# Kernel tuning notes

Measured on AMD Instinct MI355X. Metric: run time of the kernel, lower is better.

## Reference

```python
import jax, jax.numpy as jnp
import numpy as np

EPS_LN = 1e-5

def _layernorm(x, g, b):
    mu = jnp.mean(x, axis=-1, keepdims=True)
    var = jnp.mean((x - mu) ** 2, axis=-1, keepdims=True)
    return (x - mu) * jax.lax.rsqrt(var + EPS_LN) * g + b

def _act_quant_ste(x):
    # clip_val uses detached stats -> stop_gradient
    clip_val = jax.lax.stop_gradient(
        jnp.clip(jnp.mean(jnp.abs(x), axis=-1, keepdims=True), 1e-8, None)) * 2.5
    scale = clip_val / 127.0
    x_scaled = x / scale
    x_clip = jnp.clip(x_scaled, -127.0, 127.0)
    x_q = x_scaled + jax.lax.stop_gradient(jnp.round(x_clip) - x_scaled)
    return x_q * scale

def _weight_quant_ste(w):
    scale = jax.lax.stop_gradient(jnp.clip(jnp.mean(jnp.abs(w)), 1e-8, None))
    w_norm = w / scale
    w_clip = jnp.clip(w_norm, -1.0, 1.0)
    w_q = w_norm + jax.lax.stop_gradient(jnp.round(w_clip) - w_norm)
    return w_q * scale

def _bitlinear(x, w, g, b):
    # w: [out, in]; x: [B,T,in]
    x_q = _act_quant_ste(_layernorm(x, g, b))
    w_q = _weight_quant_ste(w)
    return jnp.einsum('btd,hd->bth', x_q, w_q)

def setup_inputs() -> dict:
    D, H = 2048, 2048 * 4
    B, T = 4, 2048
    key = jax.random.key(0)
    ks = jax.random.split(key, 4)
    std = 0.02
    return {
        'x': jax.random.normal(ks[0], (B, T, D), dtype=jnp.float32),
        'mu_k': jnp.zeros((1, 1, D), jnp.float32),
        'mu_r': jnp.zeros((1, 1, D), jnp.float32),
        'wk': jax.random.normal(ks[1], (H, D), jnp.float32) * std,
        'gk': jnp.ones((D,), jnp.float32), 'bk': jnp.zeros((D,), jnp.float32),
        'wr': jax.random.normal(ks[2], (D, D), jnp.float32) * std,
        'gr': jnp.ones((D,), jnp.float32), 'br': jnp.zeros((D,), jnp.float32),
        'wv': jax.random.normal(ks[3], (D, H), jnp.float32) * std,
        'gv': jnp.ones((H,), jnp.float32), 'bv': jnp.zeros((H,), jnp.float32),
    }

def reference(x, mu_k, mu_r, wk, gk, bk, wr, gr, br, wv, gv, bv):
    B, T, C = x.shape
    prev = jnp.zeros((B, 1, C), dtype=x.dtype)  # state=None path
    x_prev = jnp.concatenate([prev, x[:, :-1, :]], axis=1)  # token shift
    dx = x_prev - x
    k_act = jax.nn.relu(_bitlinear(x + dx * mu_k, wk, gk, bk)) ** 2  # [B,T,H]
    rgate = jax.nn.sigmoid(_bitlinear(x + dx * mu_r, wr, gr, br))    # [B,T,D]
    out = rgate * _bitlinear(k_act, wv, gv, bv)                      # [B,T,D]
    return out, jax.lax.stop_gradient(x[:, -1:, :])
```

## Files before the change

### kernel.cpp

```cpp
#include <hip/hip_runtime.h>

#define T_LEN 2048
#define B_SZ  4
#define D_DIM 2048
#define H_DIM 8192
#define BT    (B_SZ * T_LEN)

typedef float f32x4 __attribute__((ext_vector_type(4)));
typedef int   i32x4v __attribute__((ext_vector_type(4)));
typedef int   i32x16v __attribute__((ext_vector_type(16)));

__device__ __forceinline__ float block_sum(float v, float* red) {
    #pragma unroll
    for (int o = 32; o > 0; o >>= 1) v += __shfl_down(v, o, 64);
    const int lane = threadIdx.x & 63, w = threadIdx.x >> 6;
    if (lane == 0) red[w] = v;
    __syncthreads();
    float r = red[0] + red[1] + red[2] + red[3];
    __syncthreads();
    return r;
}

__global__ void wabs_partial(const float* __restrict__ w, int n,
                             float* __restrict__ part) {
    __shared__ float red[16];
    float s = 0.f;
    int i = (blockIdx.x * 256 + threadIdx.x) * 8;
    const int stride = gridDim.x * 256 * 8;
    for (; i < n; i += stride) {
        f32x4 a = *(const f32x4*)(w + i);
        f32x4 b = *(const f32x4*)(w + i + 4);
        #pragma unroll
        for (int j = 0; j < 4; j++) s += fabsf(a[j]) + fabsf(b[j]);
    }
    float tot = block_sum(s, red);
    if (threadIdx.x == 0) part[blockIdx.x] = tot;
}

__global__ void wfinal(const float* __restrict__ part, int nparts, int n,
                       float* __restrict__ outp) {
    __shared__ float red[16];
    float s = 0.f;
    for (int i = threadIdx.x; i < nparts; i += 256) s += part[i];
    float tot = block_sum(s, red);
    if (threadIdx.x == 0) outp[0] = fmaxf(tot / (float)n, 1e-8f);
}

__global__ void wquant(const float* __restrict__ w, const float* __restrict__ sp,
                       signed char* __restrict__ q, int n) {
    const float s = *sp;
    int i = (blockIdx.x * 256 + threadIdx.x) * 16;
    const int stride = gridDim.x * 256 * 16;
    for (; i < n; i += stride) {
        union { signed char c[16]; i32x4v v; } pk;
        #pragma unroll
        for (int h = 0; h < 4; h++) {
            f32x4 a = *(const f32x4*)(w + i + h * 4);
            #pragma unroll
            for (int j = 0; j < 4; j++)
                pk.c[h * 4 + j] =
                    (signed char)(int)rintf(fminf(fmaxf(a[j] / s, -1.f), 1.f));
        }
        *(i32x4v*)(q + i) = pk.v;
    }
}

__device__ __forceinline__ void ln_quant8(const float* xm_in,
                                          const float* __restrict__ g,
                                          const float* __restrict__ b,
                                          signed char* qrow, float* srow, float* red) {
    const int base = threadIdx.x * 8;
    float xm[8];
    float s = 0.f;
    #pragma unroll
    for (int j = 0; j < 8; j++) { xm[j] = xm_in[j]; s += xm[j]; }
    const float mean = block_sum(s, red) * (1.f / D_DIM);
    float s2 = 0.f;
    #pragma unroll
    for (int j = 0; j < 8; j++) { float d = xm[j] - mean; s2 += d * d; }
    const float var  = block_sum(s2, red) * (1.f / D_DIM);
    const float rstd = 1.f / sqrtf(var + 1e-5f);
    f32x4 ga = *(const f32x4*)(g + base), gb = *(const f32x4*)(g + base + 4);
    f32x4 ba = *(const f32x4*)(b + base), bb2 = *(const f32x4*)(b + base + 4);
    float gg[8] = {ga[0],ga[1],ga[2],ga[3],gb[0],gb[1],gb[2],gb[3]};
    float bb[8] = {ba[0],ba[1],ba[2],ba[3],bb2[0],bb2[1],bb2[2],bb2[3]};
    float sa = 0.f;
    #pragma unroll
    for (int j = 0; j < 8; j++) {
        xm[j] = (xm[j] - mean) * rstd * gg[j] + bb[j];
        sa += fabsf(xm[j]);
    }
    const float amean = block_sum(sa, red) * (1.f / D_DIM);
    const float scale = fmaxf(amean, 1e-8f) * 2.5f / 127.0f;
    union { signed char c[8]; int2 v; } pk;
    #pragma unroll
    for (int j = 0; j < 8; j++)
        pk.c[j] = (signed char)(int)rintf(fminf(fmaxf(xm[j] / scale, -127.f), 127.f));
    *(int2*)(qrow + base) = pk.v;
    if (threadIdx.x == 0) *srow = scale;
}

__global__ void act_prep(const float* __restrict__ x, int row0,
                         const float* __restrict__ muk,
                         const float* __restrict__ gk, const float* __restrict__ bk,
                         const float* __restrict__ mur,
                         const float* __restrict__ gr, const float* __restrict__ br,
                         signed char* __restrict__ qk, float* __restrict__ sk,
                         signed char* __restrict__ qr, float* __restrict__ sr,
                         float* __restrict__ out2) {
    __shared__ float red[16];
    const int lrow = blockIdx.x;
    const int row = row0 + lrow;
    const int t = row & (T_LEN - 1);
    const int base = threadIdx.x * 8;

    float xv[8], xp[8];
    f32x4 xa = *(const f32x4*)(x + (size_t)row * D_DIM + base);
    f32x4 xb = *(const f32x4*)(x + (size_t)row * D_DIM + base + 4);
    xv[0]=xa[0]; xv[1]=xa[1]; xv[2]=xa[2]; xv[3]=xa[3];
    xv[4]=xb[0]; xv[5]=xb[1]; xv[6]=xb[2]; xv[7]=xb[3];
    if (t > 0) {
        f32x4 pa = *(const f32x4*)(x + (size_t)(row - 1) * D_DIM + base);
        f32x4 pb = *(const f32x4*)(x + (size_t)(row - 1) * D_DIM + base + 4);
        xp[0]=pa[0]; xp[1]=pa[1]; xp[2]=pa[2]; xp[3]=pa[3];
        xp[4]=pb[0]; xp[5]=pb[1]; xp[6]=pb[2]; xp[7]=pb[3];
    } else {
        #pragma unroll
        for (int j = 0; j < 8; j++) xp[j] = 0.f;
    }
    if (t == T_LEN - 1) {
        const int bb = row / T_LEN;
        *(f32x4*)(out2 + (size_t)bb * D_DIM + base)     = xa;
        *(f32x4*)(out2 + (size_t)bb * D_DIM + base + 4) = xb;
    }
    float mk[8], mr[8], xmk[8], xmr[8];
    f32x4 mka = *(const f32x4*)(muk + base), mkb = *(const f32x4*)(muk + base + 4);
    f32x4 mra = *(const f32x4*)(mur + base), mrb = *(const f32x4*)(mur + base + 4);
    mk[0]=mka[0]; mk[1]=mka[1]; mk[2]=mka[2]; mk[3]=mka[3];
    mk[4]=mkb[0]; mk[5]=mkb[1]; mk[6]=mkb[2]; mk[7]=mkb[3];
    mr[0]=mra[0]; mr[1]=mra[1]; mr[2]=mra[2]; mr[3]=mra[3];
    mr[4]=mrb[0]; mr[5]=mrb[1]; mr[6]=mrb[2]; mr[7]=mrb[3];
    #pragma unroll
    for (int j = 0; j < 8; j++) {
        const float dx = xp[j] - xv[j];
        xmk[j] = xv[j] + dx * mk[j];
        xmr[j] = xv[j] + dx * mr[j];
    }
    ln_quant8(xmk, gk, bk, qk + (size_t)lrow * D_DIM, sk + lrow, red);
    ln_quant8(xmr, gr, br, qr + (size_t)lrow * D_DIM, sr + lrow, red);
}

__global__ void lnq_v(const float* __restrict__ kact,
                      const float* __restrict__ g, const float* __restrict__ b,
                      signed char* __restrict__ qv, float* __restrict__ sv) {
    __shared__ float red[16];
    const int row = blockIdx.x;
    const int base = threadIdx.x * 32;
    const float* kr = kact + (size_t)row * H_DIM + base;

    float v[32];
    float s = 0.f;
    #pragma unroll
    for (int c = 0; c < 8; c++) {
        f32x4 a = *(const f32x4*)(kr + c * 4);
        #pragma unroll
        for (int j = 0; j < 4; j++) { v[c * 4 + j] = a[j]; s += a[j]; }
    }
    const float mean = block_sum(s, red) * (1.f / H_DIM);
    float s2 = 0.f;
    #pragma unroll
    for (int j = 0; j < 32; j++) { float d = v[j] - mean; s2 += d * d; }
    const float var  = block_sum(s2, red) * (1.f / H_DIM);
    const float rstd = 1.f / sqrtf(var + 1e-5f);
    float sa = 0.f;
    #pragma unroll
    for (int c = 0; c < 8; c++) {
        f32x4 ga = *(const f32x4*)(g + base + c * 4);
        f32x4 ba = *(const f32x4*)(b + base + c * 4);
        #pragma unroll
        for (int j = 0; j < 4; j++) {
            int k = c * 4 + j;
            v[k] = (v[k] - mean) * rstd * ga[j] + ba[j];
            sa += fabsf(v[k]);
        }
    }
    const float amean = block_sum(sa, red) * (1.f / H_DIM);
    const float scale = fmaxf(amean, 1e-8f) * 2.5f / 127.0f;
    union { signed char c[32]; i32x4v v4[2]; } pk;
    #pragma unroll
    for (int j = 0; j < 32; j++)
        pk.c[j] = (signed char)(int)rintf(fminf(fmaxf(v[j] / scale, -127.f), 127.f));
    *(i32x4v*)(qv + (size_t)row * H_DIM + base)      = pk.v4[0];
    *(i32x4v*)(qv + (size_t)row * H_DIM + base + 16) = pk.v4[1];
    if (threadIdx.x == 0) sv[row] = scale;
}

template <int EP, int BM, int BN, int WM, int WN>
__global__ __launch_bounds__(512, 2) void gemm8(
    const signed char* __restrict__ A, const signed char* __restrict__ B,
    int K, int Nn, int gn,
    const float* __restrict__ sa, const float* __restrict__ swp,
    const float* __restrict__ gate, float* __restrict__ out_f) {
    constexpr int MT  = BM / WM / 32;
    constexpr int NTC = BN / WN / 32;
    constexpr int ALOADS = BM / 64;
    constexpr int BLOADS = BN / 64;
    constexpr int LOADS  = ALOADS + BLOADS;
    constexpr int L0 = LOADS / 2;

    __shared__ signed char As[2][BM * 128];
    __shared__ signed char Bs[2][BN * 128];

    const int tid = threadIdx.x;
    const int nwg = gridDim.x;
    const int q8  = nwg >> 3;
    const int swz = (blockIdx.x & 7) * q8 + (blockIdx.x >> 3);
    const int bm = swz / gn, bn = swz % gn;

    const int lane = tid & 63, wave = tid >> 6;
    const int wr = wave / WN, wc = wave % WN;
    const int lrow = lane & 31, lhalf = lane >> 5;

    i32x16v acc[MT][NTC] = {};

    const size_t arow0 = (size_t)bm * BM;
    const size_t brow0 = (size_t)bn * BN;
    const int NT = K >> 7;

    auto stage_one = [&](int buf, int k0, int j) {
        if (j < ALOADS) {
            const int o = j * 512 + tid;
            const int r = o >> 3, sl = o & 7;
            const signed char* g = A + (arow0 + r) * (size_t)K + k0 + ((sl ^ (r & 7)) * 16);
            __builtin_amdgcn_global_load_lds(
                (const __attribute__((address_space(1))) void*)g,
                (__attribute__((address_space(3))) void*)(As[buf] + o * 16), 16, 0, 0);
        } else {
            const int o = (j - ALOADS) * 512 + tid;
            const int r = o >> 3, sl = o & 7;
            const signed char* g = B + (brow0 + r) * (size_t)K + k0 + ((sl ^ (r & 7)) * 16);
            __builtin_amdgcn_global_load_lds(
                (const __attribute__((address_space(1))) void*)g,
                (__attribute__((address_space(3))) void*)(Bs[buf] + o * 16), 16, 0, 0);
        }
    };

    auto read_frags = [&](const signed char* AsB, const signed char* BsB, int ks0,
                          i32x4v (&af)[MT][2], i32x4v (&bf)[NTC][2]) {
        #pragma unroll
        for (int s = 0; s < 2; s++) {
            const int slot = (ks0 + s) * 2 + lhalf;
            #pragma unroll
            for (int tm = 0; tm < MT; tm++) {
                const int r = wr * (MT * 32) + tm * 32 + lrow;
                af[tm][s] = *(const i32x4v*)(AsB + r * 128 + ((slot ^ (r & 7)) * 16));
            }
            #pragma unroll
            for (int tn = 0; tn < NTC; tn++) {
                const int r = wc * (NTC * 32) + tn * 32 + lrow;
                bf[tn][s] = *(const i32x4v*)(BsB + r * 128 + ((slot ^ (r & 7)) * 16));
            }
        }
    };

    auto do_mfma = [&](i32x4v (&af)[MT][2], i32x4v (&bf)[NTC][2]) {
        #pragma unroll
        for (int s = 0; s < 2; s++)
            #pragma unroll
            for (int tm = 0; tm < MT; tm++)
                #pragma unroll
                for (int tn = 0; tn < NTC; tn++)
                    acc[tm][tn] = __builtin_amdgcn_mfma_i32_32x32x32_i8(
                        af[tm][s], bf[tn][s], acc[tm][tn], 0, 0, 0);
    };

    #pragma unroll
    for (int j = 0; j < LOADS; j++) stage_one(0, 0, j);

    for (int t = 0; t < NT; t++) {
        const int cur = t & 1;
        const signed char* AsB = As[cur];
        const signed char* BsB = Bs[cur];
        const int kn = (t + 1) << 7;
        const bool pf = (t + 1 < NT);

        if (pf) {
            #pragma unroll
            for (int j = 0; j < L0; j++) stage_one(cur ^ 1, kn, j);
            if constexpr (L0 == 4) asm volatile("s_waitcnt vmcnt(4)" ::: "memory");
            else                   asm volatile("s_waitcnt vmcnt(3)" ::: "memory");
        } else {
            asm volatile("s_waitcnt vmcnt(0)" ::: "memory");
        }
        __builtin_amdgcn_sched_barrier(0);
        __builtin_amdgcn_s_barrier();
        __builtin_amdgcn_sched_barrier(0);
        {
            i32x4v af[MT][2], bf[NTC][2];
            read_frags(AsB, BsB, 0, af, bf);
            __builtin_amdgcn_s_setprio(1);
            do_mfma(af, bf);
            __builtin_amdgcn_s_setprio(0);
        }
        __builtin_amdgcn_sched_barrier(0);
        __builtin_amdgcn_s_barrier();
        {
            i32x4v af[MT][2], bf[NTC][2];
            read_frags(AsB, BsB, 2, af, bf);
            if (pf) {
                #pragma unroll
                for (int j = L0; j < LOADS; j++) stage_one(cur ^ 1, kn, j);
            }
            __builtin_amdgcn_sched_barrier(0);
            __builtin_amdgcn_s_barrier();
            __builtin_amdgcn_sched_barrier(0);
            __builtin_amdgcn_s_setprio(1);
            do_mfma(af, bf);
            __builtin_amdgcn_s_setprio(0);
        }
        __builtin_amdgcn_sched_barrier(0);
        __builtin_amdgcn_s_barrier();
    }

    const float sw = *swp;
    #pragma unroll
    for (int tm = 0; tm < MT; tm++) {
        #pragma unroll
        for (int tn = 0; tn < NTC; tn++) {
            #pragma unroll
            for (int rg = 0; rg < 16; rg++) {
                const int rin  = (rg & 3) + 8 * (rg >> 2) + 4 * lhalf;
                const int grow = bm * BM + wr * (MT * 32) + tm * 32 + rin;
                const int gcol = bn * BN + wc * (NTC * 32) + tn * 32 + lrow;
                const float v = (float)acc[tm][tn][rg] * sa[grow] * sw;
                const size_t idx = (size_t)grow * Nn + gcol;
                if (EP == 0) {
                    float rv = fmaxf(v, 0.f);
                    out_f[idx] = rv * rv;
                } else if (EP == 1) {
                    out_f[idx] = 1.0f / (1.0f + expf(-v));
                } else {
                    out_f[idx] = gate[idx] * v;
                }
            }
        }
    }
}

extern "C" void kernel_launch(void* const* d_in, const int* in_sizes, int n_in,
                              void* d_out, int out_size, void* d_ws, size_t ws_size,
                              hipStream_t stream) {
    const float* x   = (const float*)d_in[0];
    const float* muk = (const float*)d_in[1];
    const float* mur = (const float*)d_in[2];
    const float* wk  = (const float*)d_in[3];
    const float* gk  = (const float*)d_in[4];
    const float* bk  = (const float*)d_in[5];
    const float* wr  = (const float*)d_in[6];
    const float* gr  = (const float*)d_in[7];
    const float* br  = (const float*)d_in[8];
    const float* wv  = (const float*)d_in[9];
    const float* gv  = (const float*)d_in[10];
    const float* bv  = (const float*)d_in[11];

    char* wsb = (char*)d_ws;
    size_t off = 0;
    auto alloc = [&](size_t bytes) -> size_t {
        size_t p = off;
        off = (off + bytes + 255) & ~(size_t)255;
        return p;
    };
    const size_t o_wqk  = alloc((size_t)H_DIM * D_DIM);
    const size_t o_wqr  = alloc((size_t)D_DIM * D_DIM);
    const size_t o_wqv  = alloc((size_t)D_DIM * H_DIM);
    const size_t o_wsc  = alloc(64);
    const size_t o_part = alloc(3 * 1024 * sizeof(float));
    const size_t fixed  = off;

    int CH = BT;
    while (CH > 256 &&
           fixed + (size_t)CH * (D_DIM + D_DIM + H_DIM + 4 * H_DIM + 4 * D_DIM + 12) + 8192 > ws_size)
        CH >>= 1;
    const size_t o_xqk  = alloc((size_t)CH * D_DIM);
    const size_t o_xqr  = alloc((size_t)CH * D_DIM);
    const size_t o_xqv  = alloc((size_t)CH * H_DIM);
    const size_t o_kact = alloc((size_t)CH * H_DIM * 4);
    const size_t o_gate = alloc((size_t)CH * D_DIM * 4);
    const size_t o_sk   = alloc((size_t)CH * 4);
    const size_t o_sr   = alloc((size_t)CH * 4);
    const size_t o_sv   = alloc((size_t)CH * 4);

    signed char* wqk = (signed char*)(wsb + o_wqk);
    signed char* wqr = (signed char*)(wsb + o_wqr);
    signed char* wqv = (signed char*)(wsb + o_wqv);
    float* wsc  = (float*)(wsb + o_wsc);
    float* part = (float*)(wsb + o_part);
    signed char* xqk = (signed char*)(wsb + o_xqk);
    signed char* xqr = (signed char*)(wsb + o_xqr);
    signed char* xqv = (signed char*)(wsb + o_xqv);
    float* kact = (float*)(wsb + o_kact);
    float* gate = (float*)(wsb + o_gate);
    float* sk = (float*)(wsb + o_sk);
    float* sr = (float*)(wsb + o_sr);
    float* sv = (float*)(wsb + o_sv);

    float* outp = (float*)d_out;
    float* out2 = outp + (size_t)BT * D_DIM;

    wabs_partial<<<1024, 256, 0, stream>>>(wk, H_DIM * D_DIM, part + 0 * 1024);
    wabs_partial<<<1024, 256, 0, stream>>>(wr, D_DIM * D_DIM, part + 1 * 1024);
    wabs_partial<<<1024, 256, 0, stream>>>(wv, D_DIM * H_DIM, part + 2 * 1024);
    wfinal<<<1, 256, 0, stream>>>(part + 0 * 1024, 1024, H_DIM * D_DIM, wsc + 0);
    wfinal<<<1, 256, 0, stream>>>(part + 1 * 1024, 1024, D_DIM * D_DIM, wsc + 1);
    wfinal<<<1, 256, 0, stream>>>(part + 2 * 1024, 1024, D_DIM * H_DIM, wsc + 2);
    wquant<<<2048, 256, 0, stream>>>(wk, wsc + 0, wqk, H_DIM * D_DIM);
    wquant<<<2048, 256, 0, stream>>>(wr, wsc + 1, wqr, D_DIM * D_DIM);
    wquant<<<2048, 256, 0, stream>>>(wv, wsc + 2, wqv, D_DIM * H_DIM);

    for (int row0 = 0; row0 < BT; row0 += CH) {
        act_prep<<<CH, 256, 0, stream>>>(x, row0, muk, gk, bk, mur, gr, br,
                                         xqk, sk, xqr, sr, out2);

        gemm8<1, 256, 128, 4, 2><<<(CH / 256) * (D_DIM / 128), 512, 0, stream>>>(
            xqr, wqr, D_DIM, D_DIM, D_DIM / 128, sr, wsc + 1,
            (const float*)nullptr, gate);

        gemm8<0, 256, 256, 2, 4><<<(CH / 256) * (H_DIM / 256), 512, 0, stream>>>(
            xqk, wqk, D_DIM, H_DIM, H_DIM / 256, sk, wsc + 0,
            (const float*)nullptr, kact);

        lnq_v<<<CH, 256, 0, stream>>>(kact, gv, bv, xqv, sv);

        gemm8<2, 256, 128, 4, 2><<<(CH / 256) * (D_DIM / 128), 512, 0, stream>>>(
            xqv, wqv, H_DIM, D_DIM, D_DIM / 128, sv, wsc + 2,
            gate, outp + (size_t)row0 * D_DIM);
    }
}
```

Measured before the change: 740.5 us.

## Store k_act as bf16 and retile the K-projection GEMM with BK=64

The intermediate relu² activation from the K-projection GEMM is now written as bf16 rather than fp32, which halves its write traffic and the read traffic in the following LayerNorm-quantize kernel. The GEMM template gains a BK parameter with a single-stage BK=64 pipeline and a matching LDS swizzle, and the K GEMM moves to 512x128 tiles with 8x1 waves. Chunk sizing now accounts for the smaller buffer and keeps a larger minimum chunk. Rounding k_act to bf16 before LayerNorm and int8 quantization can change some quantized values, and the new tile shape changes occupancy and LDS use.

```diff
diff --git a/kernel.cpp b/kernel.cpp
--- a/kernel.cpp
+++ b/kernel.cpp
@@ -9,6 +9,17 @@
 typedef float f32x4 __attribute__((ext_vector_type(4)));
 typedef int   i32x4v __attribute__((ext_vector_type(4)));
 typedef int   i32x16v __attribute__((ext_vector_type(16)));
+typedef unsigned short ushort8 __attribute__((ext_vector_type(8)));
+
+__device__ __forceinline__ float bf2f(unsigned short u) {
+    unsigned int i = ((unsigned int)u) << 16;
+    return __builtin_bit_cast(float, i);
+}
+__device__ __forceinline__ unsigned short f2bf(float f) {
+    unsigned int i = __builtin_bit_cast(unsigned int, f);
+    i += 0x7fffu + ((i >> 16) & 1u);
+    return (unsigned short)(i >> 16);
+}
 
 __device__ __forceinline__ float block_sum(float v, float* red) {
     #pragma unroll
@@ -150,21 +161,21 @@
     ln_quant8(xmr, gr, br, qr + (size_t)lrow * D_DIM, sr + lrow, red);
 }
 
-__global__ void lnq_v(const float* __restrict__ kact,
+__global__ void lnq_v(const unsigned short* __restrict__ kact,
                       const float* __restrict__ g, const float* __restrict__ b,
                       signed char* __restrict__ qv, float* __restrict__ sv) {
     __shared__ float red[16];
     const int row = blockIdx.x;
     const int base = threadIdx.x * 32;
-    const float* kr = kact + (size_t)row * H_DIM + base;
+    const unsigned short* kr = kact + (size_t)row * H_DIM + base;
 
     float v[32];
     float s = 0.f;
     #pragma unroll
-    for (int c = 0; c < 8; c++) {
-        f32x4 a = *(const f32x4*)(kr + c * 4);
-        #pragma unroll
-        for (int j = 0; j < 4; j++) { v[c * 4 + j] = a[j]; s += a[j]; }
+    for (int c = 0; c < 4; c++) {
+        ushort8 a = *(const ushort8*)(kr + c * 8);
+        #pragma unroll
+        for (int j = 0; j < 8; j++) { v[c * 8 + j] = bf2f(a[j]); s += v[c * 8 + j]; }
     }
     const float mean = block_sum(s, red) * (1.f / H_DIM);
     float s2 = 0.f;
@@ -195,21 +206,23 @@
     if (threadIdx.x == 0) sv[row] = scale;
 }
 
-template <int EP, int BM, int BN, int WM, int WN>
+template <int EP, int BM, int BN, int WM, int WN, int BK>
 __global__ __launch_bounds__(512, 2) void gemm8(
     const signed char* __restrict__ A, const signed char* __restrict__ B,
     int K, int Nn, int gn,
     const float* __restrict__ sa, const float* __restrict__ swp,
-    const float* __restrict__ gate, float* __restrict__ out_f) {
+    const float* __restrict__ gate, float* __restrict__ out_f,
+    unsigned short* __restrict__ out_bf) {
     constexpr int MT  = BM / WM / 32;
     constexpr int NTC = BN / WN / 32;
-    constexpr int ALOADS = BM / 64;
-    constexpr int BLOADS = BN / 64;
+    constexpr int SLOTS  = BK / 16;
+    constexpr int ALOADS = BM * BK / 8192;
+    constexpr int BLOADS = BN * BK / 8192;
     constexpr int LOADS  = ALOADS + BLOADS;
-    constexpr int L0 = LOADS / 2;
-
-    __shared__ signed char As[2][BM * 128];
-    __shared__ signed char Bs[2][BN * 128];
+    constexpr int WAITN  = (BK == 64) ? LOADS : LOADS / 2;
+
+    __shared__ signed char As[2][BM * BK];
+    __shared__ signed char Bs[2][BN * BK];
 
     const int tid = threadIdx.x;
     const int nwg = gridDim.x;
@@ -225,54 +238,62 @@
 
     const size_t arow0 = (size_t)bm * BM;
     const size_t brow0 = (size_t)bn * BN;
-    const int NT = K >> 7;
+    const int NT = K / BK;
+
+    auto fswz = [&](int r) -> int {
+        if constexpr (BK == 128) return r & 7;
+        else                     return (r >> 1) & 3;
+    };
 
     auto stage_one = [&](int buf, int k0, int j) {
         if (j < ALOADS) {
             const int o = j * 512 + tid;
-            const int r = o >> 3, sl = o & 7;
-            const signed char* g = A + (arow0 + r) * (size_t)K + k0 + ((sl ^ (r & 7)) * 16);
+            const int r = o / SLOTS, sl = o % SLOTS;
+            const signed char* g = A + (arow0 + r) * (size_t)K + k0 + ((sl ^ fswz(r)) * 16);
             __builtin_amdgcn_global_load_lds(
                 (const __attribute__((address_space(1))) void*)g,
                 (__attribute__((address_space(3))) void*)(As[buf] + o * 16), 16, 0, 0);
         } else {
             const int o = (j - ALOADS) * 512 + tid;
-            const int r = o >> 3, sl = o & 7;
-            const signed char* g = B + (brow0 + r) * (size_t)K + k0 + ((sl ^ (r & 7)) * 16);
+            const int r = o / SLOTS, sl = o % SLOTS;
+            const signed char* g = B + (brow0 + r) * (size_t)K + k0 + ((sl ^ fswz(r)) * 16);
             __builtin_amdgcn_global_load_lds(
                 (const __attribute__((address_space(1))) void*)g,
                 (__attribute__((address_space(3))) void*)(Bs[buf] + o * 16), 16, 0, 0);
         }
     };
 
-    auto read_frags = [&](const signed char* AsB, const signed char* BsB, int ks0,
-                          i32x4v (&af)[MT][2], i32x4v (&bf)[NTC][2]) {
-        #pragma unroll
-        for (int s = 0; s < 2; s++) {
-            const int slot = (ks0 + s) * 2 + lhalf;
+    auto read_slice = [&](const signed char* AsB, const signed char* BsB, int s,
+                          i32x4v (&af)[MT], i32x4v (&bf)[NTC]) {
+        const int slot = s * 2 + lhalf;
+        #pragma unroll
+        for (int tm = 0; tm < MT; tm++) {
+            const int r = wr * (MT * 32) + tm * 32 + lrow;
+            af[tm] = *(const i32x4v*)(AsB + r * BK + ((slot ^ fswz(r)) * 16));
+        }
+        #pragma unroll
+        for (int tn = 0; tn < NTC; tn++) {
+            const int r = wc * (NTC * 32) + tn * 32 + lrow;
+            bf[tn] = *(const i32x4v*)(BsB + r * BK + ((slot ^ fswz(r)) * 16));
+        }
+    };
+
+    auto mfma_slice = [&](i32x4v (&af)[MT], i32x4v (&bf)[NTC]) {
+        #pragma unroll
+        for (int tm = 0; tm < MT; tm++)
             #pragma unroll
-            for (int tm = 0; tm < MT; tm++) {
-                const int r = wr * (MT * 32) + tm * 32 + lrow;
-                af[tm][s] = *(const i32x4v*)(AsB + r * 128 + ((slot ^ (r & 7)) * 16));
-            }
-            #pragma unroll
-            for (int tn = 0; tn < NTC; tn++) {
-                const int r = wc * (NTC * 32) + tn * 32 + lrow;
-                bf[tn][s] = *(const i32x4v*)(BsB + r * 128 + ((slot ^ (r & 7)) * 16));
-            }
-        }
+            for (int tn = 0; tn < NTC; tn++)
+                acc[tm][tn] = __builtin_amdgcn_mfma_i32_32x32x32_i8(
+                    af[tm], bf[tn], acc[tm][tn], 0, 0, 0);
     };
 
-    auto do_mfma = [&](i32x4v (&af)[MT][2], i32x4v (&bf)[NTC][2]) {
-        #pragma unroll
-        for (int s = 0; s < 2; s++)
-            #pragma unroll
-            for (int tm = 0; tm < MT; tm++)
-                #pragma unroll
-                for (int tn = 0; tn < NTC; tn++)
-                    acc[tm][tn] = __builtin_amdgcn_mfma_i32_32x32x32_i8(
-                        af[tm][s], bf[tn][s], acc[tm][tn], 0, 0, 0);
-    };
+    #define WAIT_CNT()  do { \
+        if constexpr (WAITN == 2)      asm volatile("s_waitcnt vmcnt(2)" ::: "memory"); \
+        else if constexpr (WAITN == 3) asm volatile("s_waitcnt vmcnt(3)" ::: "memory"); \
+        else if constexpr (WAITN == 4) asm volatile("s_waitcnt vmcnt(4)" ::: "memory"); \
+        else if constexpr (WAITN == 5) asm volatile("s_waitcnt vmcnt(5)" ::: "memory"); \
+        else                           asm volatile("s_waitcnt vmcnt(6)" ::: "memory"); \
+    } while (0)
 
     #pragma unroll
     for (int j = 0; j < LOADS; j++) stage_one(0, 0, j);
@@ -281,46 +302,74 @@
         const int cur = t & 1;
         const signed char* AsB = As[cur];
         const signed char* BsB = Bs[cur];
-        const int kn = (t + 1) << 7;
+        const int kn = (t + 1) * BK;
         const bool pf = (t + 1 < NT);
 
-        if (pf) {
-            #pragma unroll
-            for (int j = 0; j < L0; j++) stage_one(cur ^ 1, kn, j);
-            if constexpr (L0 == 4) asm volatile("s_waitcnt vmcnt(4)" ::: "memory");
-            else                   asm volatile("s_waitcnt vmcnt(3)" ::: "memory");
-        } else {
-            asm volatile("s_waitcnt vmcnt(0)" ::: "memory");
-        }
-        __builtin_amdgcn_sched_barrier(0);
-        __builtin_amdgcn_s_barrier();
-        __builtin_amdgcn_sched_barrier(0);
-        {
-            i32x4v af[MT][2], bf[NTC][2];
-            read_frags(AsB, BsB, 0, af, bf);
-            __builtin_amdgcn_s_setprio(1);
-            do_mfma(af, bf);
-            __builtin_amdgcn_s_setprio(0);
-        }
-        __builtin_amdgcn_sched_barrier(0);
-        __builtin_amdgcn_s_barrier();
-        {
-            i32x4v af[MT][2], bf[NTC][2];
-            read_frags(AsB, BsB, 2, af, bf);
+        if constexpr (BK == 64) {
             if (pf) {
                 #pragma unroll
-                for (int j = L0; j < LOADS; j++) stage_one(cur ^ 1, kn, j);
+                for (int j = 0; j < LOADS; j++) stage_one(cur ^ 1, kn, j);
+                WAIT_CNT();
+            } else {
+                asm volatile("s_waitcnt vmcnt(0)" ::: "memory");
             }
             __builtin_amdgcn_sched_barrier(0);
             __builtin_amdgcn_s_barrier();
             __builtin_amdgcn_sched_barrier(0);
-            __builtin_amdgcn_s_setprio(1);
-            do_mfma(af, bf);
-            __builtin_amdgcn_s_setprio(0);
-        }
-        __builtin_amdgcn_sched_barrier(0);
-        __builtin_amdgcn_s_barrier();
-    }
+            {
+                i32x4v a0[MT], b0[NTC], a1[MT], b1[NTC];
+                read_slice(AsB, BsB, 0, a0, b0);
+                read_slice(AsB, BsB, 1, a1, b1);
+                __builtin_amdgcn_s_setprio(1);
+                mfma_slice(a0, b0);
+                mfma_slice(a1, b1);
+                __builtin_amdgcn_s_setprio(0);
+            }
+            __builtin_amdgcn_sched_barrier(0);
+            __builtin_amdgcn_s_barrier();
+        } else {
+            if (pf) {
+                #pragma unroll
+                for (int j = 0; j < LOADS / 2; j++) stage_one(cur ^ 1, kn, j);
+                WAIT_CNT();
+            } else {
+                asm volatile("s_waitcnt vmcnt(0)" ::: "memory");
+            }
+            __builtin_amdgcn_sched_barrier(0);
+            __builtin_amdgcn_s_barrier();
+            __builtin_amdgcn_sched_barrier(0);
+            {
+                i32x4v a0[MT], b0[NTC], a1[MT], b1[NTC];
+                read_slice(AsB, BsB, 0, a0, b0);
+                read_slice(AsB, BsB, 1, a1, b1);
+                __builtin_amdgcn_s_setprio(1);
+                mfma_slice(a0, b0);
+                mfma_slice(a1, b1);
+                __builtin_amdgcn_s_setprio(0);
+            }
+            __builtin_amdgcn_sched_barrier(0);
+            __builtin_amdgcn_s_barrier();
+            {
+                i32x4v a0[MT], b0[NTC], a1[MT], b1[NTC];
+                read_slice(AsB, BsB, 2, a0, b0);
+                read_slice(AsB, BsB, 3, a1, b1);
+                if (pf) {
+                    #pragma unroll
+                    for (int j = LOADS / 2; j < LOADS; j++) stage_one(cur ^ 1, kn, j);
+                }
+                __builtin_amdgcn_sched_barrier(0);
+                __builtin_amdgcn_s_barrier();
+                __builtin_amdgcn_sched_barrier(0);
+                __builtin_amdgcn_s_setprio(1);
+                mfma_slice(a0, b0);
+                mfma_slice(a1, b1);
+                __builtin_amdgcn_s_setprio(0);
+            }
+            __builtin_amdgcn_sched_barrier(0);
+            __builtin_amdgcn_s_barrier();
+        }
+    }
+    #undef WAIT_CNT
 
     const float sw = *swp;
     #pragma unroll
@@ -336,7 +385,7 @@
                 const size_t idx = (size_t)grow * Nn + gcol;
                 if (EP == 0) {
                     float rv = fmaxf(v, 0.f);
-                    out_f[idx] = rv * rv;
+                    out_bf[idx] = f2bf(rv * rv);
                 } else if (EP == 1) {
                     out_f[idx] = 1.0f / (1.0f + expf(-v));
                 } else {
@@ -378,13 +427,13 @@
     const size_t fixed  = off;
 
     int CH = BT;
-    while (CH > 256 &&
-           fixed + (size_t)CH * (D_DIM + D_DIM + H_DIM + 4 * H_DIM + 4 * D_DIM + 12) + 8192 > ws_size)
+    while (CH > 512 &&
+           fixed + (size_t)CH * (D_DIM + D_DIM + H_DIM + 2 * H_DIM + 4 * D_DIM + 12) + 8192 > ws_size)
         CH >>= 1;
     const size_t o_xqk  = alloc((size_t)CH * D_DIM);
     const size_t o_xqr  = alloc((size_t)CH * D_DIM);
     const size_t o_xqv  = alloc((size_t)CH * H_DIM);
-    const size_t o_kact = alloc((size_t)CH * H_DIM * 4);
+    const size_t o_kact = alloc((size_t)CH * H_DIM * 2);
     const size_t o_gate = alloc((size_t)CH * D_DIM * 4);
     const size_t o_sk   = alloc((size_t)CH * 4);
     const size_t o_sr   = alloc((size_t)CH * 4);
@@ -398,7 +447,7 @@
     signed char* xqk = (signed char*)(wsb + o_xqk);
     signed char* xqr = (signed char*)(wsb + o_xqr);
     signed char* xqv = (signed char*)(wsb + o_xqv);
-    float* kact = (float*)(wsb + o_kact);
+    unsigned short* kact = (unsigned short*)(wsb + o_kact);
     float* gate = (float*)(wsb + o_gate);
     float* sk = (float*)(wsb + o_sk);
     float* sr = (float*)(wsb + o_sr);
@@ -421,18 +470,18 @@
         act_prep<<<CH, 256, 0, stream>>>(x, row0, muk, gk, bk, mur, gr, br,
                                          xqk, sk, xqr, sr, out2);
 
-        gemm8<1, 256, 128, 4, 2><<<(CH / 256) * (D_DIM / 128), 512, 0, stream>>>(
+        gemm8<1, 256, 128, 4, 2, 128><<<(CH / 256) * (D_DIM / 128), 512, 0, stream>>>(
             xqr, wqr, D_DIM, D_DIM, D_DIM / 128, sr, wsc + 1,
-            (const float*)nullptr, gate);
-
-        gemm8<0, 256, 256, 2, 4><<<(CH / 256) * (H_DIM / 256), 512, 0, stream>>>(
-            xqk, wqk, D_DIM, H_DIM, H_DIM / 256, sk, wsc + 0,
-            (const float*)nullptr, kact);
+            (const float*)nullptr, gate, (unsigned short*)nullptr);
+
+        gemm8<0, 512, 128, 8, 1, 64><<<(CH / 512) * (H_DIM / 128), 512, 0, stream>>>(
+            xqk, wqk, D_DIM, H_DIM, H_DIM / 128, sk, wsc + 0,
+            (const float*)nullptr, (float*)nullptr, kact);
 
         lnq_v<<<CH, 256, 0, stream>>>(kact, gv, bv, xqv, sv);
 
-        gemm8<2, 256, 128, 4, 2><<<(CH / 256) * (D_DIM / 128), 512, 0, stream>>>(
+        gemm8<2, 256, 128, 4, 2, 128><<<(CH / 256) * (D_DIM / 128), 512, 0, stream>>>(
             xqv, wqv, H_DIM, D_DIM, D_DIM / 128, sv, wsc + 2,
-            gate, outp + (size_t)row0 * D_DIM);
-    }
-}
+            gate, outp + (size_t)row0 * D_DIM, (unsigned short*)nullptr);
+    }
+}
```

Result: faster. 692.3 us (-6.5%).
